# Kernel tuning notes

Hardware: AMD Instinct MI355X
Metric: run time of the kernel (lower is better)

Reference implementation:

```python
import jax, jax.numpy as jnp
import numpy as np

HEADS = 12
D_MODEL = 768
D_K = D_MODEL // HEADS


def setup_inputs() -> dict:
    key = jax.random.key(0)
    ks = jax.random.split(key, 11)
    B, S, D = 2, 2048, D_MODEL
    s = 1.0 / np.sqrt(D)
    return {
        "query": jax.random.normal(ks[0], (B, S, D), jnp.float32),
        "key": jax.random.normal(ks[1], (B, S, D), jnp.float32),
        "value": jax.random.normal(ks[2], (B, S, D), jnp.float32),
        "Wq": jax.random.normal(ks[3], (D, D), jnp.float32) * s,
        "bq": jnp.zeros((D,), jnp.float32),
        "Wk": jax.random.normal(ks[4], (D, D), jnp.float32) * s,
        "bk": jnp.zeros((D,), jnp.float32),
        "Wv": jax.random.normal(ks[5], (D, D), jnp.float32) * s,
        "bv": jnp.zeros((D,), jnp.float32),
        "Wo": jax.random.normal(ks[6], (D, D), jnp.float32) * s,
        "bo": jnp.zeros((D,), jnp.float32),
    }


def reference(query, key, value, Wq, bq, Wk, bk, Wv, bv, Wo, bo):
    B, S, D = query.shape
    # linear projections (weights stored as [in, out])
    q = query @ Wq + bq
    k = key @ Wk + bk
    v = value @ Wv + bv
    # [B, H, S, d_k]
    q = q.reshape(B, S, HEADS, D_K).transpose(0, 2, 1, 3)
    k = k.reshape(B, S, HEADS, D_K).transpose(0, 2, 1, 3)
    v = v.reshape(B, S, HEADS, D_K).transpose(0, 2, 1, 3)
    # scores: note module scales by sqrt(d_k) (key.size(-1)), not self.scaled
    scores = jnp.einsum("bhqd,bhkd->bhqk", q, k) / jnp.sqrt(jnp.asarray(D_K, q.dtype))
    weights = jax.nn.softmax(scores, axis=-1)
    context = jnp.einsum("bhqk,bhkd->bhqd", weights, v)
    context = context.transpose(0, 2, 1, 3).reshape(B, S, D)
    return context @ Wo + bo
```

## Files before the change

kernel.cpp:

```cpp
#include <hip/hip_runtime.h>
#include <hip/hip_bf16.h>
#include <math.h>

#define D_MODEL 768
#define HEADS 12
#define DK 64
#define SEQ 2048
#define BATCH 2
#define MTOT (BATCH * SEQ)
#define QSCALE 0.18033688011112042f

using short8 = __attribute__((ext_vector_type(8))) short;
using us4    = __attribute__((ext_vector_type(4))) unsigned short;
using us8    = __attribute__((ext_vector_type(8))) unsigned short;
using f32x4  = __attribute__((ext_vector_type(4))) float;
using f32x16 = __attribute__((ext_vector_type(16))) float;

static __device__ __forceinline__ unsigned f2bf2(float x, float y) {
    __hip_bfloat162 t = __float22bfloat162_rn(float2{x, y});
    return *reinterpret_cast<unsigned*>(&t);
}
static __device__ __forceinline__ unsigned short f2bf1(float x) {
    __hip_bfloat16 t = __float2bfloat16(x);
    return *reinterpret_cast<unsigned short*>(&t);
}
static __device__ __forceinline__ float bf2f(unsigned short u) {
    unsigned v = (unsigned)u << 16;
    return __uint_as_float(v);
}
static __device__ __forceinline__ short8 cvt8(float4 a, float4 b) {
    union { unsigned u[4]; short8 s; } r;
    r.u[0] = f2bf2(a.x, a.y);
    r.u[1] = f2bf2(a.z, a.w);
    r.u[2] = f2bf2(b.x, b.y);
    r.u[3] = f2bf2(b.z, b.w);
    return r.s;
}
static __device__ __forceinline__ float fast_exp2(float x) {
#if __has_builtin(__builtin_amdgcn_exp2f)
    return __builtin_amdgcn_exp2f(x);
#else
    return __expf(x * 0.6931471805599453f);
#endif
}
static __device__ __forceinline__ unsigned pk2(float lo, float hi) {
    unsigned d;
    asm("v_cvt_pk_bf16_f32 %0, %1, %2" : "=v"(d) : "v"(lo), "v"(hi));
    return d;
}

static __device__ __forceinline__ void gload_lds16(const void* g, void* l) {
    __builtin_amdgcn_global_load_lds(
        (const __attribute__((address_space(1))) void*)g,
        (__attribute__((address_space(3))) void*)l, 16, 0, 0);
}

static __device__ __forceinline__ void barrier_lgkm() {
    asm volatile("s_waitcnt lgkmcnt(0)" ::: "memory");
    __builtin_amdgcn_s_barrier();
    __builtin_amdgcn_sched_barrier(0);
}
static __device__ __forceinline__ void barrier_vm0() {
    asm volatile("s_waitcnt vmcnt(0)" ::: "memory");
    __builtin_amdgcn_s_barrier();
    __builtin_amdgcn_sched_barrier(0);
}

__global__ __launch_bounds__(256) void cvt_wt_k(
    const float* __restrict__ Wq, const float* __restrict__ Wk,
    const float* __restrict__ Wv, const float* __restrict__ Wo,
    unsigned short* __restrict__ Wqt, unsigned short* __restrict__ Wkt,
    unsigned short* __restrict__ Wvt, unsigned short* __restrict__ Wot)
{
    const int z = blockIdx.z;
    const float* W = z == 0 ? Wq : z == 1 ? Wk : z == 2 ? Wv : Wo;
    unsigned short* Wt = z == 0 ? Wqt : z == 1 ? Wkt : z == 2 ? Wvt : Wot;
    __shared__ float t[32][33];
    const int n0 = blockIdx.x * 32, k0 = blockIdx.y * 32;
    const int tx = threadIdx.x & 31;
    const int ty0 = (threadIdx.x >> 5) * 4;
    #pragma unroll
    for (int j = 0; j < 4; ++j)
        t[ty0 + j][tx] = W[(size_t)(k0 + ty0 + j) * D_MODEL + n0 + tx];
    __syncthreads();
    #pragma unroll
    for (int j = 0; j < 4; ++j)
        Wt[(size_t)(n0 + ty0 + j) * D_MODEL + k0 + tx] = f2bf1(t[tx][ty0 + j]);
}

__global__ __launch_bounds__(512) void gemm_qkv_k(
    const float* __restrict__ query, const float* __restrict__ key,
    const float* __restrict__ value,
    const unsigned short* __restrict__ Wqt, const unsigned short* __restrict__ Wkt,
    const unsigned short* __restrict__ Wvt,
    const float* __restrict__ bq, const float* __restrict__ bk,
    const float* __restrict__ bv,
    unsigned short* __restrict__ qb, unsigned short* __restrict__ kb,
    unsigned short* __restrict__ vb)
{
    __shared__ __align__(16) char gsm[65536];

    const int bid = blockIdx.x;
    const int xcd = bid & 7;
    const int idx = bid >> 3;
    const int z   = idx / 24;
    const int rr  = idx % 24;
    const int brow = (xcd * 4 + rr / 6) * 128;
    const int bcol = (rr % 6) * 128;

    const float* A           = z == 0 ? query : z == 1 ? key : value;
    const unsigned short* Wt = z == 0 ? Wqt : z == 1 ? Wkt : Wvt;
    const float* bias        = z == 0 ? bq  : z == 1 ? bk  : bv;
    unsigned short* C        = z == 0 ? qb  : z == 1 ? kb  : vb;
    const float scale        = z == 0 ? QSCALE : 1.0f;

    const int tid  = threadIdx.x;
    const int w    = tid >> 6;
    const int lane = tid & 63;
    const int g    = lane >> 4, c = lane & 15;
    const int wr   = w >> 2, wc = w & 3;

    f32x4 acc[4][2] = {};

    const int xc  = (c & 7) << 4;
    const int rb0 = c * 128 + ((g * 16) ^ xc);
    const int rb1 = c * 128 + ((64 + g * 16) ^ xc);

    const int ar = tid >> 2;
    const int ac = (tid & 3) << 4;
    int awa[2];
    #pragma unroll
    for (int i = 0; i < 2; ++i)
        awa[i] = ar * 128 + (((ac << 1) + 16 * i) ^ ((ar & 7) << 4));
    const float* Ap32 = A + (size_t)(brow + ar) * D_MODEL + ac;

    const int br2 = tid >> 2;
    const int bs2 = (tid & 3) << 1;
    int bwa[2];
    #pragma unroll
    for (int i = 0; i < 2; ++i)
        bwa[i] = 32768 + br2 * 128 + (((bs2 + i) ^ (br2 & 7)) << 4);
    const unsigned short* WtB = Wt + (size_t)(bcol + br2) * D_MODEL + bs2 * 8;

    float4 rA0[4], rA1[4];
    us8    rB0[2], rB1[2];

    auto loadA0 = [&](int k0) {
        rA0[0] = *(const float4*)(Ap32 + k0);
        rA0[1] = *(const float4*)(Ap32 + k0 + 4);
        rA0[2] = *(const float4*)(Ap32 + k0 + 8);
        rA0[3] = *(const float4*)(Ap32 + k0 + 12);
    };
    auto loadA1 = [&](int k0) {
        rA1[0] = *(const float4*)(Ap32 + k0);
        rA1[1] = *(const float4*)(Ap32 + k0 + 4);
        rA1[2] = *(const float4*)(Ap32 + k0 + 8);
        rA1[3] = *(const float4*)(Ap32 + k0 + 12);
    };
    auto loadB0 = [&](int k0) {
        rB0[0] = *(const us8*)(WtB + k0);
        rB0[1] = *(const us8*)(WtB + k0 + 8);
    };
    auto loadB1 = [&](int k0) {
        rB1[0] = *(const us8*)(WtB + k0);
        rB1[1] = *(const us8*)(WtB + k0 + 8);
    };
    auto writeA0 = [&](int buf) {
        *(short8*)(gsm + buf * 16384 + awa[0]) = cvt8(rA0[0], rA0[1]);
        *(short8*)(gsm + buf * 16384 + awa[1]) = cvt8(rA0[2], rA0[3]);
    };
    auto writeA1 = [&](int buf) {
        *(short8*)(gsm + buf * 16384 + awa[0]) = cvt8(rA1[0], rA1[1]);
        *(short8*)(gsm + buf * 16384 + awa[1]) = cvt8(rA1[2], rA1[3]);
    };
    auto writeB0 = [&](int buf) {
        *(us8*)(gsm + buf * 16384 + bwa[0]) = rB0[0];
        *(us8*)(gsm + buf * 16384 + bwa[1]) = rB0[1];
    };
    auto writeB1 = [&](int buf) {
        *(us8*)(gsm + buf * 16384 + bwa[0]) = rB1[0];
        *(us8*)(gsm + buf * 16384 + bwa[1]) = rB1[1];
    };

    loadA0(0);  loadB0(0);
    loadA1(64); loadB1(64);
    writeA0(0); writeB0(0);
    barrier_lgkm();

    for (int iter = 0; iter < 6; ++iter) {
        #pragma unroll
        for (int u = 0; u < 2; ++u) {
            const int n   = 2 * iter + u;
            const int kb2 = min(n + 2, 11) * 64;
            if (u == 0) { loadA0(kb2); loadB0(kb2); }
            else        { loadA1(kb2); loadB1(kb2); }
            __builtin_amdgcn_sched_barrier(0);

            __builtin_amdgcn_s_setprio(1);
            #pragma unroll
            for (int kstep = 0; kstep < 2; ++kstep) {
                const int rb = kstep ? rb1 : rb0;
                short8 af[4], bf[2];
                #pragma unroll
                for (int m = 0; m < 4; ++m)
                    af[m] = *(const short8*)(gsm + u * 16384 + wr * 8192 +
                                             m * 2048 + rb);
                #pragma unroll
                for (int nn = 0; nn < 2; ++nn)
                    bf[nn] = *(const short8*)(gsm + 32768 + u * 16384 +
                                              wc * 4096 + nn * 2048 + rb);
                #pragma unroll
                for (int m = 0; m < 4; ++m)
                    #pragma unroll
                    for (int nn = 0; nn < 2; ++nn)
                        acc[m][nn] = __builtin_amdgcn_mfma_f32_16x16x32_bf16(
                                         af[m], bf[nn], acc[m][nn], 0, 0, 0);
            }
            __builtin_amdgcn_s_setprio(0);
            __builtin_amdgcn_sched_barrier(0);

            if (u == 0) { writeA1(1); writeB1(1); }
            else        { writeA0(0); writeB0(0); }
            barrier_lgkm();
        }
    }

    #pragma unroll
    for (int m = 0; m < 4; ++m)
        #pragma unroll
        for (int n = 0; n < 2; ++n) {
            const int col = bcol + wc * 32 + n * 16 + c;
            const float bval = bias[col];
            #pragma unroll
            for (int j = 0; j < 4; ++j) {
                const int row = brow + wr * 64 + m * 16 + g * 4 + j;
                C[(size_t)row * D_MODEL + col] = f2bf1((acc[m][n][j] + bval) * scale);
            }
        }
}

__global__ __launch_bounds__(256) void gemm_o_k(
    const unsigned short* __restrict__ A, const unsigned short* __restrict__ Wt,
    const float* __restrict__ bias, float* __restrict__ C)
{
    __shared__ __align__(16) char gsm[32768];

    const int bid = blockIdx.x;
    const int xcd = bid & 7;
    const int idx = bid >> 3;
    const int brow = (xcd * 8 + idx / 12) * 64;
    const int bcol = (idx % 12) * 64;

    const int tid  = threadIdx.x;
    const int w    = tid >> 6;
    const int lane = tid & 63;
    const int g    = lane >> 4, c = lane & 15;
    const int wr   = w >> 1, wc = w & 1;

    f32x4 acc[2][2] = {{f32x4{0,0,0,0}, f32x4{0,0,0,0}},
                       {f32x4{0,0,0,0}, f32x4{0,0,0,0}}};

    const int xc  = (c & 7) << 4;
    const int rb0 = c * 128 + ((g * 16) ^ xc);
    const int rb1 = c * 128 + ((64 + g * 16) ^ xc);
    const int a0 = rb0 + wr * 4096, a1 = rb1 + wr * 4096;
    const int b0r = rb0 + 16384 + wc * 4096, b1r = rb1 + 16384 + wc * 4096;

    int bsrow[2], bsoff[2], bsdst[2];
    #pragma unroll
    for (int r = 0; r < 2; ++r) {
        int phys = (w + 4 * r) * 1024 + lane * 16;
        int row  = phys >> 7;
        int slot = (phys >> 4) & 7;
        bsrow[r] = row;
        bsoff[r] = (slot ^ (row & 7)) * 8;
        bsdst[r] = (w + 4 * r) * 1024;
    }

    auto stage = [&](int k0, int buf) {
        #pragma unroll
        for (int r = 0; r < 2; ++r) {
            gload_lds16(A  + (size_t)(brow + bsrow[r]) * D_MODEL + k0 + bsoff[r],
                        gsm + buf * 8192 + bsdst[r]);
            gload_lds16(Wt + (size_t)(bcol + bsrow[r]) * D_MODEL + k0 + bsoff[r],
                        gsm + 16384 + buf * 8192 + bsdst[r]);
        }
    };

    stage(0, 0);
    barrier_vm0();

    for (int k0 = 0; k0 < D_MODEL; k0 += 128) {
        #pragma unroll
        for (int u = 0; u < 2; ++u) {
            const int kn = min(k0 + u * 64 + 64, D_MODEL - 64);
            stage(kn, u ^ 1);
            __builtin_amdgcn_sched_barrier(0);

            #pragma unroll
            for (int kstep = 0; kstep < 2; ++kstep) {
                short8 af[2], bf[2];
                #pragma unroll
                for (int m = 0; m < 2; ++m)
                    af[m] = *(const short8*)(gsm + u * 8192 + m * 2048 +
                                             (kstep ? a1 : a0));
                #pragma unroll
                for (int n = 0; n < 2; ++n)
                    bf[n] = *(const short8*)(gsm + u * 8192 + n * 2048 +
                                             (kstep ? b1r : b0r));
                #pragma unroll
                for (int m = 0; m < 2; ++m)
                    #pragma unroll
                    for (int n = 0; n < 2; ++n)
                        acc[m][n] = __builtin_amdgcn_mfma_f32_16x16x32_bf16(
                                        af[m], bf[n], acc[m][n], 0, 0, 0);
            }
            barrier_vm0();
        }
    }

    #pragma unroll
    for (int m = 0; m < 2; ++m)
        #pragma unroll
        for (int n = 0; n < 2; ++n) {
            const int col = bcol + wc * 32 + n * 16 + c;
            const float bval = bias[col];
            #pragma unroll
            for (int j = 0; j < 4; ++j) {
                const int row = brow + wr * 32 + m * 16 + g * 4 + j;
                C[(size_t)row * D_MODEL + col] = acc[m][n][j] + bval;
            }
        }
}

__global__ __launch_bounds__(256) void attn_mfma_k(
    const unsigned short* __restrict__ q, const unsigned short* __restrict__ k,
    const unsigned short* __restrict__ v, unsigned short* __restrict__ opart,
    float* __restrict__ mpart, float* __restrict__ lpart)
{
    __shared__ __align__(16) char sm[32768];

    const int tid  = threadIdx.x;
    const int w    = tid >> 6;
    const int lane = tid & 63;
    const int c    = lane & 31;
    const int hi   = lane >> 5;

    const int bid  = blockIdx.x;
    const int swz  = (bid & 7) * 96 + (bid >> 3);
    const int qt   = swz & 15;
    const int rest = swz >> 4;
    const int half = rest & 1;
    const int hb   = rest >> 1;
    const int h    = hb % HEADS;
    const int b    = hb / HEADS;
    const int q0   = qt * 128;
    const int NT2  = 16;

    short8 qf[4];
    {
        const unsigned short* qp =
            q + (size_t)(b * SEQ + q0 + w * 32 + c) * D_MODEL + h * DK;
        #pragma unroll
        for (int t = 0; t < 4; ++t)
            qf[t] = *(const short8*)(qp + t * 16 + hi * 8);
    }

    float m_run = -INFINITY;
    f32x16 lacc = {};
    f32x16 o0 = {}, o1 = {};
    const short8 ONES = {0x3F80, 0x3F80, 0x3F80, 0x3F80,
                         0x3F80, 0x3F80, 0x3F80, 0x3F80};

    const int xc = (c & 7) << 4;
    int koff[4];
    #pragma unroll
    for (int t = 0; t < 4; ++t)
        koff[t] = ((32 * t + 16 * hi) ^ xc) + c * 128;

    int kdst[2];
    const unsigned short* kg[2];
    {
        const unsigned short* kbase =
            k + (size_t)(b * SEQ + half * (SEQ / 2)) * D_MODEL + h * DK;
        #pragma unroll
        for (int r = 0; r < 2; ++r) {
            int phys = (w + 4 * r) * 1024 + lane * 16;
            int row  = phys >> 7;
            int slot = (phys >> 4) & 7;
            kdst[r]  = (w + 4 * r) * 1024;
            kg[r]    = kbase + (size_t)row * D_MODEL + (slot ^ (row & 7)) * 8;
        }
    }
    const int cv = tid & 15, vd0 = (tid >> 4) << 2;
    const int vposP = 16 * (cv >> 3) + 8 * ((cv >> 2) & 1) + 2 * (cv & 3);
    int vwa[4];
    #pragma unroll
    for (int j = 0; j < 4; ++j) {
        const int row = vd0 + j;
        vwa[j] = 16384 + row * 128 + ((2 * vposP) ^ ((row & 7) << 4));
    }
    const unsigned short* vg =
        v + (size_t)(b * SEQ + half * (SEQ / 2) + cv) * D_MODEL + h * DK + vd0;
    const int TS = 64 * D_MODEL;

    us4 va, vb_, vc, vd;

    auto issue_k = [&](int buf) {
        gload_lds16(kg[0], sm + buf * 8192 + kdst[0]);
        gload_lds16(kg[1], sm + buf * 8192 + kdst[1]);
        kg[0] += TS; kg[1] += TS;
    };
    auto load_v = [&]() {
        va  = *(const us4*)(vg);
        vb_ = *(const us4*)(vg + 16 * D_MODEL);
        vc  = *(const us4*)(vg + 32 * D_MODEL);
        vd  = *(const us4*)(vg + 48 * D_MODEL);
        vg += TS;
    };
    auto write_v = [&](int buf) {
        #pragma unroll
        for (int j = 0; j < 4; ++j) {
            unsigned lo  = (unsigned)va[j]  | ((unsigned)vc[j] << 16);
            unsigned hi2 = (unsigned)vb_[j] | ((unsigned)vd[j] << 16);
            *(unsigned*)(sm + buf * 8192 + vwa[j])        = lo;
            *(unsigned*)(sm + buf * 8192 + (vwa[j] ^ 64)) = hi2;
        }
    };

    issue_k(0);
    __builtin_amdgcn_sched_barrier(0);
    load_v();
    write_v(0);
    barrier_lgkm();

    for (int kt2 = 0; kt2 < NT2; kt2 += 2) {
        #pragma unroll
        for (int u = 0; u < 2; ++u) {
            const int tile = kt2 + u;
            issue_k(u ^ 1);
            __builtin_amdgcn_sched_barrier(0);
            load_v();
            __builtin_amdgcn_sched_barrier(0);

            f32x16 s0 = {}, s1 = {};
            __builtin_amdgcn_s_setprio(1);
            #pragma unroll
            for (int t = 0; t < 4; ++t) {
                short8 kf0 = *(const short8*)(sm + u * 8192 + koff[t]);
                short8 kf1 = *(const short8*)(sm + u * 8192 + 4096 + koff[t]);
                s0 = __builtin_amdgcn_mfma_f32_32x32x16_bf16(kf0, qf[t], s0, 0, 0, 0);
                s1 = __builtin_amdgcn_mfma_f32_32x32x16_bf16(kf1, qf[t], s1, 0, 0, 0);
            }
            __builtin_amdgcn_s_setprio(0);

            float rmax = s0[0];
            #pragma unroll
            for (int r = 1; r < 16; ++r) rmax = fmaxf(rmax, s0[r]);
            #pragma unroll
            for (int r = 0; r < 16; ++r) rmax = fmaxf(rmax, s1[r]);
            rmax = fmaxf(rmax, __shfl_xor(rmax, 32));

            if (tile == 0) {
                m_run = rmax;
            } else if (__any(rmax > m_run + 11.0f)) {
                const float mnew = fmaxf(m_run, rmax);
                const float sc = fast_exp2(m_run - mnew);
                m_run = mnew;
                #pragma unroll
                for (int r = 0; r < 16; ++r) {
                    const float scr = __shfl(sc, (r & 3) + 8 * (r >> 2) + 4 * hi);
                    lacc[r] *= scr;
                    o0[r] *= scr;
                    o1[r] *= scr;
                }
            }

            #pragma unroll
            for (int r = 0; r < 16; ++r) {
                s0[r] = fast_exp2(s0[r] - m_run);
                s1[r] = fast_exp2(s1[r] - m_run);
            }

            __builtin_amdgcn_s_setprio(1);
            #pragma unroll
            for (int t = 0; t < 4; ++t) {
                union { unsigned u4[4]; short8 s8; } pf;
                #pragma unroll
                for (int j = 0; j < 4; ++j)
                    pf.u4[j] = pk2(s0[4 * t + j], s1[4 * t + j]);
                short8 vf0 = *(const short8*)(sm + 16384 + u * 8192 + koff[t]);
                short8 vf1 = *(const short8*)(sm + 16384 + u * 8192 + 4096 + koff[t]);
                lacc = __builtin_amdgcn_mfma_f32_32x32x16_bf16(pf.s8, ONES, lacc, 0, 0, 0);
                o0 = __builtin_amdgcn_mfma_f32_32x32x16_bf16(pf.s8, vf0, o0, 0, 0, 0);
                o1 = __builtin_amdgcn_mfma_f32_32x32x16_bf16(pf.s8, vf1, o1, 0, 0, 0);
            }
            __builtin_amdgcn_s_setprio(0);

            write_v(u ^ 1);
            barrier_lgkm();
        }
    }

    const size_t obase = (size_t)half * ((size_t)MTOT * D_MODEL) +
                         (size_t)(b * SEQ) * D_MODEL + h * DK;
    #pragma unroll
    for (int r = 0; r < 16; ++r) {
        const int qrow = q0 + w * 32 + (r & 3) + 8 * (r >> 2) + 4 * hi;
        unsigned short* ob = opart + obase + (size_t)qrow * D_MODEL;
        ob[c]      = f2bf1(o0[r]);
        ob[32 + c] = f2bf1(o1[r]);
    }
    const size_t mlbase = (size_t)half * MTOT * HEADS +
                          (size_t)(b * SEQ) * HEADS + h;
    if (hi == 0)
        mpart[mlbase + (size_t)(q0 + w * 32 + c) * HEADS] = m_run;
    if (c == 0) {
        #pragma unroll
        for (int r = 0; r < 16; ++r) {
            const int qrow = q0 + w * 32 + (r & 3) + 8 * (r >> 2) + 4 * hi;
            lpart[mlbase + (size_t)qrow * HEADS] = lacc[r];
        }
    }
}

__global__ __launch_bounds__(256) void combine_k(
    const unsigned short* __restrict__ op, const float* __restrict__ mp,
    const float* __restrict__ lp, unsigned short* __restrict__ cb)
{
    const int t   = blockIdx.x * 256 + threadIdx.x;
    const int row = t / 96;
    const int gi  = t - row * 96;
    const int col = gi << 3;
    const int h   = gi >> 3;

    const float m0 = mp[(size_t)row * HEADS + h];
    const float m1 = mp[(size_t)MTOT * HEADS + (size_t)row * HEADS + h];
    const float l0 = lp[(size_t)row * HEADS + h];
    const float l1 = lp[(size_t)MTOT * HEADS + (size_t)row * HEADS + h];
    const float m  = fmaxf(m0, m1);
    const float s0 = fast_exp2(m0 - m);
    const float s1 = fast_exp2(m1 - m);
    const float inv = 1.0f / (l0 * s0 + l1 * s1);
    const float a0 = s0 * inv, a1 = s1 * inv;

    const size_t off = (size_t)row * D_MODEL + col;
    us4 x0  = *(const us4*)(op + off);
    us4 x0b = *(const us4*)(op + off + 4);
    us4 x1  = *(const us4*)(op + (size_t)MTOT * D_MODEL + off);
    us4 x1b = *(const us4*)(op + (size_t)MTOT * D_MODEL + off + 4);

    union { unsigned short u[8]; short8 s; } r;
    #pragma unroll
    for (int j = 0; j < 4; ++j) {
        r.u[j]     = f2bf1(bf2f(x0[j])  * a0 + bf2f(x1[j])  * a1);
        r.u[4 + j] = f2bf1(bf2f(x0b[j]) * a0 + bf2f(x1b[j]) * a1);
    }
    *(short8*)(cb + off) = r.s;
}

extern "C" void kernel_launch(void* const* d_in, const int* in_sizes, int n_in,
                              void* d_out, int out_size, void* d_ws, size_t ws_size,
                              hipStream_t stream) {
    const float* query = (const float*)d_in[0];
    const float* key   = (const float*)d_in[1];
    const float* value = (const float*)d_in[2];
    const float* Wq = (const float*)d_in[3];
    const float* bq = (const float*)d_in[4];
    const float* Wk = (const float*)d_in[5];
    const float* bk = (const float*)d_in[6];
    const float* Wv = (const float*)d_in[7];
    const float* bv = (const float*)d_in[8];
    const float* Wo = (const float*)d_in[9];
    const float* bo = (const float*)d_in[10];
    float* out = (float*)d_out;

    const size_t mat = (size_t)MTOT * D_MODEL;
    unsigned short* qb  = (unsigned short*)d_ws;
    unsigned short* kb  = qb + mat;
    unsigned short* vb  = kb + mat;
    unsigned short* cb  = vb + mat;
    unsigned short* Wqt = cb + mat;
    unsigned short* Wkt = Wqt + (size_t)D_MODEL * D_MODEL;
    unsigned short* Wvt = Wkt + (size_t)D_MODEL * D_MODEL;
    unsigned short* Wot = Wvt + (size_t)D_MODEL * D_MODEL;
    unsigned short* op  = Wot + (size_t)D_MODEL * D_MODEL;
    float*          mp  = (float*)(op + 2 * mat);
    float*          lp  = mp + 2 * (size_t)MTOT * HEADS;

    cvt_wt_k<<<dim3(D_MODEL / 32, D_MODEL / 32, 4), 256, 0, stream>>>(
        Wq, Wk, Wv, Wo, Wqt, Wkt, Wvt, Wot);

    gemm_qkv_k<<<dim3(576), 512, 0, stream>>>(
        query, key, value, Wqt, Wkt, Wvt, bq, bk, bv, qb, kb, vb);

    attn_mfma_k<<<dim3(768), 256, 0, stream>>>(qb, kb, vb, op, mp, lp);

    combine_k<<<dim3(MTOT * D_MODEL / 8 / 256), 256, 0, stream>>>(op, mp, lp, cb);

    gemm_o_k<<<dim3(768), 256, 0, stream>>>(cb, Wot, bo, out);
}
```

Measured before the change: 102.8 us.

## Replace direct global-to-LDS loads with register-staged prefetch two tiles ahead in output GEMM

The output-projection GEMM no longer uses global_load_lds with a full vmcnt(0) wait per tile. It now loads tiles into registers two k-steps ahead, writes them to swizzled LDS after the MFMAs, and synchronizes with an lgkmcnt-only barrier. The aim is to hide global-memory latency behind compute instead of stalling on every tile. It also raises wave priority around the MFMA block. The cost is extra VGPRs and explicit LDS store instructions.

```diff
diff --git a/kernel.cpp b/kernel.cpp
--- a/kernel.cpp
+++ b/kernel.cpp
@@ -57,11 +57,6 @@
 
 static __device__ __forceinline__ void barrier_lgkm() {
     asm volatile("s_waitcnt lgkmcnt(0)" ::: "memory");
-    __builtin_amdgcn_s_barrier();
-    __builtin_amdgcn_sched_barrier(0);
-}
-static __device__ __forceinline__ void barrier_vm0() {
-    asm volatile("s_waitcnt vmcnt(0)" ::: "memory");
     __builtin_amdgcn_s_barrier();
     __builtin_amdgcn_sched_barrier(0);
 }
@@ -266,37 +261,53 @@
     const int a0 = rb0 + wr * 4096, a1 = rb1 + wr * 4096;
     const int b0r = rb0 + 16384 + wc * 4096, b1r = rb1 + 16384 + wc * 4096;
 
-    int bsrow[2], bsoff[2], bsdst[2];
-    #pragma unroll
-    for (int r = 0; r < 2; ++r) {
-        int phys = (w + 4 * r) * 1024 + lane * 16;
-        int row  = phys >> 7;
-        int slot = (phys >> 4) & 7;
-        bsrow[r] = row;
-        bsoff[r] = (slot ^ (row & 7)) * 8;
-        bsdst[r] = (w + 4 * r) * 1024;
-    }
-
-    auto stage = [&](int k0, int buf) {
-        #pragma unroll
-        for (int r = 0; r < 2; ++r) {
-            gload_lds16(A  + (size_t)(brow + bsrow[r]) * D_MODEL + k0 + bsoff[r],
-                        gsm + buf * 8192 + bsdst[r]);
-            gload_lds16(Wt + (size_t)(bcol + bsrow[r]) * D_MODEL + k0 + bsoff[r],
-                        gsm + 16384 + buf * 8192 + bsdst[r]);
-        }
-    };
-
-    stage(0, 0);
-    barrier_vm0();
-
-    for (int k0 = 0; k0 < D_MODEL; k0 += 128) {
+    const int r2 = tid >> 2;
+    const int s2 = (tid & 3) << 1;
+    int wa[2];
+    #pragma unroll
+    for (int i = 0; i < 2; ++i)
+        wa[i] = r2 * 128 + (((s2 + i) ^ (r2 & 7)) << 4);
+    const unsigned short* Ap = A  + (size_t)(brow + r2) * D_MODEL + s2 * 8;
+    const unsigned short* Bp = Wt + (size_t)(bcol + r2) * D_MODEL + s2 * 8;
+
+    us8 rA0[2], rA1[2], rB0[2], rB1[2];
+
+    auto loadA0 = [&](int k0) { rA0[0] = *(const us8*)(Ap + k0); rA0[1] = *(const us8*)(Ap + k0 + 8); };
+    auto loadA1 = [&](int k0) { rA1[0] = *(const us8*)(Ap + k0); rA1[1] = *(const us8*)(Ap + k0 + 8); };
+    auto loadB0 = [&](int k0) { rB0[0] = *(const us8*)(Bp + k0); rB0[1] = *(const us8*)(Bp + k0 + 8); };
+    auto loadB1 = [&](int k0) { rB1[0] = *(const us8*)(Bp + k0); rB1[1] = *(const us8*)(Bp + k0 + 8); };
+    auto writeA0 = [&](int buf) {
+        *(us8*)(gsm + buf * 8192 + wa[0]) = rA0[0];
+        *(us8*)(gsm + buf * 8192 + wa[1]) = rA0[1];
+    };
+    auto writeA1 = [&](int buf) {
+        *(us8*)(gsm + buf * 8192 + wa[0]) = rA1[0];
+        *(us8*)(gsm + buf * 8192 + wa[1]) = rA1[1];
+    };
+    auto writeB0 = [&](int buf) {
+        *(us8*)(gsm + 16384 + buf * 8192 + wa[0]) = rB0[0];
+        *(us8*)(gsm + 16384 + buf * 8192 + wa[1]) = rB0[1];
+    };
+    auto writeB1 = [&](int buf) {
+        *(us8*)(gsm + 16384 + buf * 8192 + wa[0]) = rB1[0];
+        *(us8*)(gsm + 16384 + buf * 8192 + wa[1]) = rB1[1];
+    };
+
+    loadA0(0);  loadB0(0);
+    loadA1(64); loadB1(64);
+    writeA0(0); writeB0(0);
+    barrier_lgkm();
+
+    for (int iter = 0; iter < 6; ++iter) {
         #pragma unroll
         for (int u = 0; u < 2; ++u) {
-            const int kn = min(k0 + u * 64 + 64, D_MODEL - 64);
-            stage(kn, u ^ 1);
+            const int n   = 2 * iter + u;
+            const int kb2 = min(n + 2, 11) * 64;
+            if (u == 0) { loadA0(kb2); loadB0(kb2); }
+            else        { loadA1(kb2); loadB1(kb2); }
             __builtin_amdgcn_sched_barrier(0);
 
+            __builtin_amdgcn_s_setprio(1);
             #pragma unroll
             for (int kstep = 0; kstep < 2; ++kstep) {
                 short8 af[2], bf[2];
@@ -305,17 +316,22 @@
                     af[m] = *(const short8*)(gsm + u * 8192 + m * 2048 +
                                              (kstep ? a1 : a0));
                 #pragma unroll
-                for (int n = 0; n < 2; ++n)
-                    bf[n] = *(const short8*)(gsm + u * 8192 + n * 2048 +
-                                             (kstep ? b1r : b0r));
+                for (int nn = 0; nn < 2; ++nn)
+                    bf[nn] = *(const short8*)(gsm + u * 8192 + nn * 2048 +
+                                              (kstep ? b1r : b0r));
                 #pragma unroll
                 for (int m = 0; m < 2; ++m)
                     #pragma unroll
-                    for (int n = 0; n < 2; ++n)
-                        acc[m][n] = __builtin_amdgcn_mfma_f32_16x16x32_bf16(
-                                        af[m], bf[n], acc[m][n], 0, 0, 0);
-            }
-            barrier_vm0();
+                    for (int nn = 0; nn < 2; ++nn)
+                        acc[m][nn] = __builtin_amdgcn_mfma_f32_16x16x32_bf16(
+                                         af[m], bf[nn], acc[m][nn], 0, 0, 0);
+            }
+            __builtin_amdgcn_s_setprio(0);
+            __builtin_amdgcn_sched_barrier(0);
+
+            if (u == 0) { writeA1(1); writeB1(1); }
+            else        { writeA0(0); writeB0(0); }
+            barrier_lgkm();
         }
     }
 
```

Result: no change. 103.6 us (+0.8%).
